# Kernel optimization log

Measured on AMD Instinct MI355X. Metric: run time of the kernel, lower is better.

## Reference

```python
import jax, jax.numpy as jnp
import numpy as np

T, B, V, H, EMB, L = 64, 32, 32000, 1024, 512, 2
PAD, COPY_ID = 0, 3
EPS = 1e-07


def setup_inputs() -> dict:
    key = jax.random.key(0)
    ks = jax.random.split(key, 20)
    s = lambda k, shape, fan: jax.random.normal(k, shape, jnp.float32) / np.sqrt(fan)
    E = s(ks[0], (V, EMB), EMB).at[PAD].set(0.0)  # padding_idx row zero
    return {
        'ref_tokens': jax.random.randint(ks[1], (T, B), 0, V, jnp.int32),
        'h0': jax.random.normal(ks[2], (L, B, H), jnp.float32),
        'c0': jax.random.normal(ks[3], (L, B, H), jnp.float32),
        'E': E,
        'W_ih0': s(ks[4], (4 * H, EMB + H), EMB + H),
        'W_hh0': s(ks[5], (4 * H, H), H),
        'b_ih0': s(ks[6], (4 * H,), H),
        'b_hh0': s(ks[7], (4 * H,), H),
        'W_ih1': s(ks[8], (4 * H, H), H),
        'W_hh1': s(ks[9], (4 * H, H), H),
        'b_ih1': s(ks[10], (4 * H,), H),
        'b_hh1': s(ks[11], (4 * H,), H),
        'Wk': s(ks[12], (H, H), H),
        'bk': s(ks[13], (H,), H),
        'Wc': s(ks[14], (H, 2 * H), 2 * H),
        'bc': s(ks[15], (H,), H),
        'Wp': s(ks[16], (V, H), H),
        'bp': s(ks[17], (V,), H),
    }


def _lstm_cell(x, h, c, Wih, Whh, bih, bhh):
    g = x @ Wih.T + bih + h @ Whh.T + bhh
    i, f, gg, o = jnp.split(g, 4, axis=-1)
    c2 = jax.nn.sigmoid(f) * c + jax.nn.sigmoid(i) * jnp.tanh(gg)
    h2 = jax.nn.sigmoid(o) * jnp.tanh(c2)
    return h2, c2


def _decode(ref_tokens, h0, c0, E, W_ih0, W_hh0, b_ih0, b_hh0,
            W_ih1, W_hh1, b_ih1, b_hh1, Wk, bk, Wc, bc, Wp, bp):
    pad_mask = (ref_tokens == PAD).astype(jnp.float32)      # [T,B]
    b_idx = jnp.broadcast_to(jnp.arange(B)[None, :], (T, B))
    pos = jnp.arange(T)

    def step(carry, xt):
        feed, h, c, hbuf = carry          # feed [B,H], h/c [L,B,H], hbuf [T,B,H]
        tok, t = xt
        emb = E[tok]                      # [B,EMB]
        x = jnp.concatenate([emb, feed], axis=1)
        h0_, c0_ = _lstm_cell(x, h[0], c[0], W_ih0, W_hh0, b_ih0, b_hh0)
        h1_, c1_ = _lstm_cell(h0_, h[1], c[1], W_ih1, W_hh1, b_ih1, b_hh1)
        htop = h1_                        # [B,H]
        hbuf = hbuf.at[t].set(htop)
        # self attention over hiddens 0..t
        keyv = hbuf @ Wk.T + bk           # [T,B,H]
        scores = (keyv * htop[None]).sum(-1) + pad_mask * -99999.0
        scores = jnp.where(pos[:, None] <= t, scores, -1e30)
        dist = jax.nn.softmax(scores, axis=0)          # [T,B]
        summary = (hbuf * dist[:, :, None]).sum(0)     # [B,H]
        comb = jnp.concatenate([htop, summary], axis=1) @ Wc.T + bc  # [B,H]
        pred_logits = comb @ Wp.T + bp                 # [B,V]
        pred_probs = jax.nn.softmax(pred_logits, axis=1)
        copy_probs = jnp.zeros((B, V), jnp.float32).at[(b_idx, ref_tokens)].add(dist) + EPS
        cw = pred_probs[:, COPY_ID:COPY_ID + 1]
        out = jnp.log(cw * copy_probs + (1.0 - cw) * pred_probs)
        new_h = jnp.stack([h0_, h1_])
        new_c = jnp.stack([c0_, c1_])
        return (comb, new_h, new_c, hbuf), out

    init = (jnp.zeros((B, H), jnp.float32), h0, c0, jnp.zeros((T, B, H), jnp.float32))
    (_, hT, cT, _), preds = jax.lax.scan(step, init, (ref_tokens, pos))
    return preds  # [T,B,V]


def reference(ref_tokens, h0, c0, E, W_ih0, W_hh0, b_ih0, b_hh0,
              W_ih1, W_hh1, b_ih1, b_hh1, Wk, bk, Wc, bc, Wp, bp):
    return _decode(ref_tokens, h0, c0, E, W_ih0, W_hh0, b_ih0, b_hh0,
                   W_ih1, W_hh1, b_ih1, b_hh1, Wk, bk, Wc, bc, Wp, bp)
```

## Files before the change

### kernel.cpp

```cpp
#include <hip/hip_runtime.h>
#include <math.h>

#define T_ 64
#define B_ 32
#define V_ 32000
#define H_ 1024
#define EMB_ 512
#define EPS_ 1e-7f
#define COPY_ID_ 3

typedef __bf16 bf16x8 __attribute__((ext_vector_type(8)));
typedef float f32x4 __attribute__((ext_vector_type(4)));

__device__ __forceinline__ unsigned short f2bf(float x) {
    union { float f; unsigned int i; } v; v.f = x;
    unsigned int r = v.i + 0x7FFF + ((v.i >> 16) & 1);
    return (unsigned short)(r >> 16);
}
__device__ __forceinline__ float bf2f(unsigned short h) {
    union { unsigned int i; float f; } v; v.i = ((unsigned int)h) << 16;
    return v.f;
}
__device__ __forceinline__ void f2hilo(float v, unsigned short& h, unsigned short& l) {
    h = f2bf(v);
    l = f2bf(v - bf2f(h));
}

__global__ __launch_bounds__(256) void pack_gates_kernel(
    const float* __restrict__ Wih, int Kih, const float* __restrict__ Whh,
    int Kout, unsigned short* __restrict__ hi, unsigned short* __restrict__ lo)
{
    int idx = blockIdx.x * 256 + threadIdx.x;
    int kq = Kout >> 2;
    int jp = idx / kq;
    if (jp >= 4096) return;
    int k = (idx - jp * kq) << 2;
    int j = (jp & 3) * H_ + (jp >> 2);
    float4 v = (k < Kih) ? *(const float4*)(Wih + (size_t)j * Kih + k)
                         : *(const float4*)(Whh + (size_t)j * H_ + (k - Kih));
    unsigned short h0,l0,h1,l1,h2,l2,h3,l3;
    f2hilo(v.x,h0,l0); f2hilo(v.y,h1,l1); f2hilo(v.z,h2,l2); f2hilo(v.w,h3,l3);
    ushort4 vh; vh.x=h0; vh.y=h1; vh.z=h2; vh.w=h3;
    ushort4 vl; vl.x=l0; vl.y=l1; vl.z=l2; vl.w=l3;
    ((ushort4*)hi)[idx] = vh;
    ((ushort4*)lo)[idx] = vl;
}

__global__ __launch_bounds__(256) void pack_plain_kernel(
    const float* __restrict__ W, unsigned short* __restrict__ hi,
    unsigned short* __restrict__ lo, int n4)
{
    int idx = blockIdx.x * 256 + threadIdx.x;
    if (idx >= n4) return;
    float4 v = ((const float4*)W)[idx];
    unsigned short h0,l0,h1,l1,h2,l2,h3,l3;
    f2hilo(v.x,h0,l0); f2hilo(v.y,h1,l1); f2hilo(v.z,h2,l2); f2hilo(v.w,h3,l3);
    ushort4 vh; vh.x=h0; vh.y=h1; vh.z=h2; vh.w=h3;
    ushort4 vl; vl.x=l0; vl.y=l1; vl.z=l2; vl.w=l3;
    ((ushort4*)hi)[idx] = vh;
    ((ushort4*)lo)[idx] = vl;
}

__global__ __launch_bounds__(256) void embed_hilo_kernel(
    const float* __restrict__ E, const int* __restrict__ tok,
    unsigned short* __restrict__ Xh, unsigned short* __restrict__ Xl)
{
    int idx = blockIdx.x * 256 + threadIdx.x;
    int row = idx >> 7, k = (idx & 127) << 2;
    int tv = tok[row];
    float4 v = *(const float4*)(E + (size_t)tv * EMB_ + k);
    unsigned short h0,l0,h1,l1,h2,l2,h3,l3;
    f2hilo(v.x,h0,l0); f2hilo(v.y,h1,l1); f2hilo(v.z,h2,l2); f2hilo(v.w,h3,l3);
    ushort4 vh; vh.x=h0; vh.y=h1; vh.z=h2; vh.w=h3;
    ushort4 vl; vl.x=l0; vl.y=l1; vl.z=l2; vl.w=l3;
    ((ushort4*)Xh)[idx] = vh;
    ((ushort4*)Xl)[idx] = vl;
}

__global__ __launch_bounds__(256) void init_states_kernel(
    const float* __restrict__ h0i,
    unsigned short* __restrict__ x0h, unsigned short* __restrict__ x0l,
    unsigned short* __restrict__ x1h, unsigned short* __restrict__ x1l)
{
    int idx = blockIdx.x * 256 + threadIdx.x;
    int b = idx >> 10, u = idx & 1023;
    unsigned short h, l;
    x0h[b*2048 + u] = 0; x0l[b*2048 + u] = 0;
    f2hilo(h0i[idx], h, l);
    x0h[b*2048 + 1024 + u] = h; x0l[b*2048 + 1024 + u] = l;
    x1h[b*2048 + u] = 0; x1l[b*2048 + u] = 0;
    f2hilo(h0i[32768 + idx], h, l);
    x1h[b*2048 + 1024 + u] = h; x1l[b*2048 + 1024 + u] = l;
}

template<int K, int XE>
__global__ __launch_bounds__(256) void lstm_mfma_kernel(
    const unsigned short* __restrict__ Xe_h, const unsigned short* __restrict__ Xe_l,
    const unsigned short* __restrict__ Xr_h, const unsigned short* __restrict__ Xr_l,
    const unsigned short* __restrict__ Wh,  const unsigned short* __restrict__ Wl,
    const float* __restrict__ bih, const float* __restrict__ bhh,
    float* __restrict__ c_io,
    unsigned short* __restrict__ d1h, unsigned short* __restrict__ d1l, int d1s, int d1o,
    unsigned short* __restrict__ d2h, unsigned short* __restrict__ d2l, int d2s, int d2o,
    float* __restrict__ hf32)
{
    const int tid = threadIdx.x;
    const int wave = tid >> 6, lane = tid & 63;
    const int quad = lane >> 4, l15 = lane & 15;
    const int n0 = blockIdx.x * 16;
    constexpr int Kq = K >> 2;
    const int kb = wave * Kq;
    const int col = quad * 8;
    f32x4 acc0 = {0.f,0.f,0.f,0.f}, acc1 = {0.f,0.f,0.f,0.f};
    const unsigned short* wrh = Wh + (size_t)(n0 + l15) * K + kb + col;
    const unsigned short* wrl = Wl + (size_t)(n0 + l15) * K + kb + col;
    #pragma unroll 4
    for (int ks = 0; ks < Kq; ks += 32) {
        const int k = kb + ks;
        const unsigned short *ah, *al; int as_;
        if (XE != 0 && k < XE) { ah = Xe_h + k + col; al = Xe_l + k + col; as_ = EMB_; }
        else                   { ah = Xr_h + (k - XE) + col; al = Xr_l + (k - XE) + col; as_ = 2048; }
        bf16x8 a0h = *(const bf16x8*)(ah + l15 * as_);
        bf16x8 a0l = *(const bf16x8*)(al + l15 * as_);
        bf16x8 a1h = *(const bf16x8*)(ah + (16 + l15) * as_);
        bf16x8 a1l = *(const bf16x8*)(al + (16 + l15) * as_);
        bf16x8 bh  = *(const bf16x8*)(wrh + ks);
        bf16x8 bl  = *(const bf16x8*)(wrl + ks);
        acc0 = __builtin_amdgcn_mfma_f32_16x16x32_bf16(a0h, bh, acc0, 0, 0, 0);
        acc1 = __builtin_amdgcn_mfma_f32_16x16x32_bf16(a1h, bh, acc1, 0, 0, 0);
        acc0 = __builtin_amdgcn_mfma_f32_16x16x32_bf16(a0h, bl, acc0, 0, 0, 0);
        acc1 = __builtin_amdgcn_mfma_f32_16x16x32_bf16(a1h, bl, acc1, 0, 0, 0);
        acc0 = __builtin_amdgcn_mfma_f32_16x16x32_bf16(a0l, bh, acc0, 0, 0, 0);
        acc1 = __builtin_amdgcn_mfma_f32_16x16x32_bf16(a1l, bh, acc1, 0, 0, 0);
    }
    __shared__ float Gs[4][32][16];
    __shared__ float Gr[32][16];
    #pragma unroll
    for (int rr = 0; rr < 4; rr++) {
        Gs[wave][quad * 4 + rr][l15]      = acc0[rr];
        Gs[wave][16 + quad * 4 + rr][l15] = acc1[rr];
    }
    __syncthreads();
    #pragma unroll
    for (int it = 0; it < 2; it++) {
        int idx = tid + it * 256;
        int b = idx >> 4, nl = idx & 15;
        float g = Gs[0][b][nl] + Gs[1][b][nl] + Gs[2][b][nl] + Gs[3][b][nl];
        int jn = n0 + nl;
        int j = (jn & 3) * H_ + (jn >> 2);
        Gr[b][nl] = g + bih[j] + bhh[j];
    }
    __syncthreads();
    if (tid < 128) {
        const int b = tid & 31, ul = tid >> 5;
        const int u = (n0 >> 2) + ul;
        const float gi = Gr[b][ul * 4 + 0];
        const float gf = Gr[b][ul * 4 + 1];
        const float gg = Gr[b][ul * 4 + 2];
        const float go = Gr[b][ul * 4 + 3];
        const float cold = c_io[b * H_ + u];
        const float si = 1.f / (1.f + __expf(-gi));
        const float sf = 1.f / (1.f + __expf(-gf));
        const float so = 1.f / (1.f + __expf(-go));
        const float cn = sf * cold + si * tanhf(gg);
        const float hn = so * tanhf(cn);
        c_io[b * H_ + u] = cn;
        unsigned short hh, hl;
        f2hilo(hn, hh, hl);
        d1h[b * d1s + d1o + u] = hh;
        d1l[b * d1s + d1o + u] = hl;
        d2h[b * d2s + d2o + u] = hh;
        d2l[b * d2s + d2o + u] = hl;
        if (hf32) hf32[b * H_ + u] = hn;
    }
}

template<int K, int MODE>
__global__ __launch_bounds__(256) void gemm32_mfma_kernel(
    const unsigned short* __restrict__ Xh, const unsigned short* __restrict__ Xl,
    const unsigned short* __restrict__ Wh, const unsigned short* __restrict__ Wl,
    const float* __restrict__ bias,
    float* __restrict__ outf, unsigned short* __restrict__ outbf,
    unsigned short* __restrict__ dh, unsigned short* __restrict__ dl)
{
    const int tid = threadIdx.x;
    const int wave = tid >> 6, lane = tid & 63;
    const int quad = lane >> 4, l15 = lane & 15;
    const int n0 = blockIdx.x * 16;
    constexpr int Kq = K >> 2;
    const int kb = wave * Kq;
    const int col = quad * 8;
    f32x4 acc0 = {0.f,0.f,0.f,0.f}, acc1 = {0.f,0.f,0.f,0.f};
    const unsigned short* x0h = Xh + (size_t)l15 * K + kb + col;
    const unsigned short* x0l = Xl + (size_t)l15 * K + kb + col;
    const unsigned short* x1h = Xh + (size_t)(16 + l15) * K + kb + col;
    const unsigned short* x1l = Xl + (size_t)(16 + l15) * K + kb + col;
    const unsigned short* wrh = Wh + (size_t)(n0 + l15) * K + kb + col;
    const unsigned short* wrl = Wl + (size_t)(n0 + l15) * K + kb + col;
    #pragma unroll 4
    for (int ks = 0; ks < Kq; ks += 32) {
        bf16x8 a0h = *(const bf16x8*)(x0h + ks);
        bf16x8 a0l = *(const bf16x8*)(x0l + ks);
        bf16x8 a1h = *(const bf16x8*)(x1h + ks);
        bf16x8 a1l = *(const bf16x8*)(x1l + ks);
        bf16x8 bh  = *(const bf16x8*)(wrh + ks);
        bf16x8 bl  = *(const bf16x8*)(wrl + ks);
        acc0 = __builtin_amdgcn_mfma_f32_16x16x32_bf16(a0h, bh, acc0, 0, 0, 0);
        acc1 = __builtin_amdgcn_mfma_f32_16x16x32_bf16(a1h, bh, acc1, 0, 0, 0);
        acc0 = __builtin_amdgcn_mfma_f32_16x16x32_bf16(a0h, bl, acc0, 0, 0, 0);
        acc1 = __builtin_amdgcn_mfma_f32_16x16x32_bf16(a1h, bl, acc1, 0, 0, 0);
        acc0 = __builtin_amdgcn_mfma_f32_16x16x32_bf16(a0l, bh, acc0, 0, 0, 0);
        acc1 = __builtin_amdgcn_mfma_f32_16x16x32_bf16(a1l, bh, acc1, 0, 0, 0);
    }
    __shared__ float Gs[4][32][16];
    #pragma unroll
    for (int rr = 0; rr < 4; rr++) {
        Gs[wave][quad * 4 + rr][l15]      = acc0[rr];
        Gs[wave][16 + quad * 4 + rr][l15] = acc1[rr];
    }
    __syncthreads();
    #pragma unroll
    for (int it = 0; it < 2; it++) {
        int idx = tid + it * 256;
        int b = idx >> 4, nl = idx & 15;
        int n = n0 + nl;
        float v = Gs[0][b][nl] + Gs[1][b][nl] + Gs[2][b][nl] + Gs[3][b][nl] + bias[n];
        if (MODE == 0) {
            outf[b * H_ + n] = v;
        } else {
            outbf[b * H_ + n] = f2bf(v);
            unsigned short hh, hl;
            f2hilo(v, hh, hl);
            dh[b * 2048 + n] = hh;
            dl[b * 2048 + n] = hl;
        }
    }
}

__global__ __launch_bounds__(256) void attn_kernel(
    int t, const float* __restrict__ hbuf, const float* __restrict__ keybuf,
    const int* __restrict__ tokens, float* __restrict__ dist_all,
    unsigned short* __restrict__ cat_h, unsigned short* __restrict__ cat_l)
{
    const int bb = blockIdx.x;
    const int tid = threadIdx.x;
    __shared__ float ht[H_];
    __shared__ float sc[T_];
    __shared__ float dsh[T_];
    for (int k = tid; k < H_; k += 256)
        ht[k] = hbuf[((size_t)t * B_ + bb) * H_ + k];
    __syncthreads();
    const int wave = tid >> 6, lane = tid & 63;
    for (int s = wave; s <= t; s += 4) {
        const float* kv = keybuf + ((size_t)s * B_ + bb) * H_;
        float p = 0.f;
        #pragma unroll
        for (int j = 0; j < 16; j++) p += kv[lane + 64 * j] * ht[lane + 64 * j];
        #pragma unroll
        for (int off = 32; off > 0; off >>= 1) p += __shfl_down(p, off, 64);
        if (lane == 0) {
            float pen = (tokens[s * B_ + bb] == 0) ? -99999.0f : 0.0f;
            sc[s] = p + pen;
        }
    }
    __syncthreads();
    if (tid < 64) {
        float v = (tid <= t) ? sc[tid] : -1e30f;
        float m = v;
        #pragma unroll
        for (int off = 32; off > 0; off >>= 1) m = fmaxf(m, __shfl_down(m, off, 64));
        m = __shfl(m, 0, 64);
        float e = (tid <= t) ? __expf(v - m) : 0.f;
        float ss = e;
        #pragma unroll
        for (int off = 32; off > 0; off >>= 1) ss += __shfl_down(ss, off, 64);
        ss = __shfl(ss, 0, 64);
        float d = e / ss;
        dsh[tid] = d;
        if (tid <= t) dist_all[((size_t)t * T_ + tid) * B_ + bb] = d;
    }
    __syncthreads();
    float sm0 = 0.f, sm1 = 0.f, sm2 = 0.f, sm3 = 0.f;
    for (int s = 0; s <= t; s++) {
        const float d = dsh[s];
        const float* hr = hbuf + ((size_t)s * B_ + bb) * H_;
        sm0 += d * hr[tid];
        sm1 += d * hr[tid + 256];
        sm2 += d * hr[tid + 512];
        sm3 += d * hr[tid + 768];
    }
    const int base = bb * 2048;
    unsigned short hh, hl;
    f2hilo(ht[tid],       hh, hl); cat_h[base + tid]        = hh; cat_l[base + tid]        = hl;
    f2hilo(ht[tid + 256], hh, hl); cat_h[base + tid + 256]  = hh; cat_l[base + tid + 256]  = hl;
    f2hilo(ht[tid + 512], hh, hl); cat_h[base + tid + 512]  = hh; cat_l[base + tid + 512]  = hl;
    f2hilo(ht[tid + 768], hh, hl); cat_h[base + tid + 768]  = hh; cat_l[base + tid + 768]  = hl;
    f2hilo(sm0, hh, hl); cat_h[base + 1024 + tid]       = hh; cat_l[base + 1024 + tid]       = hl;
    f2hilo(sm1, hh, hl); cat_h[base + 1024 + tid + 256] = hh; cat_l[base + 1024 + tid + 256] = hl;
    f2hilo(sm2, hh, hl); cat_h[base + 1024 + tid + 512] = hh; cat_l[base + 1024 + tid + 512] = hl;
    f2hilo(sm3, hh, hl); cat_h[base + 1024 + tid + 768] = hh; cat_l[base + 1024 + tid + 768] = hl;
}

__global__ __launch_bounds__(256) void cast_bf16_kernel(
    const float* __restrict__ src, unsigned short* __restrict__ dst, int n4)
{
    int idx = blockIdx.x * 256 + threadIdx.x;
    int stride = gridDim.x * 256;
    for (int i = idx; i < n4; i += stride) {
        float4 v = ((const float4*)src)[i];
        ushort4 o;
        o.x = f2bf(v.x); o.y = f2bf(v.y); o.z = f2bf(v.z); o.w = f2bf(v.w);
        ((ushort4*)dst)[i] = o;
    }
}

__global__ __launch_bounds__(256) void logits_mfma_kernel(
    const __bf16* __restrict__ Abf, const __bf16* __restrict__ Bbf,
    const float* __restrict__ bp, float* __restrict__ out)
{
    __shared__ __align__(16) __bf16 As[128 * 32];
    __shared__ __align__(16) __bf16 Bs[128 * 32];
    const int tid = threadIdx.x;
    const int lane = tid & 63;
    const int wave = tid >> 6;
    const int quad = lane >> 4, l15 = lane & 15;
    const int m0 = blockIdx.y * 128, n0 = blockIdx.x * 128;
    const int wm = wave >> 1, wn = wave & 1;
    const f32x4 vzero = {0.f, 0.f, 0.f, 0.f};
    f32x4 acc[4][4];
    #pragma unroll
    for (int mt = 0; mt < 4; mt++)
        #pragma unroll
        for (int nt = 0; nt < 4; nt++) acc[mt][nt] = vzero;

    for (int k0 = 0; k0 < 1024; k0 += 32) {
        #pragma unroll
        for (int i = 0; i < 2; i++) {
            int idx = i * 256 + tid;
            int row = idx >> 2, co = (idx & 3) * 8;
            ((uint4*)As)[idx] = *(const uint4*)(Abf + (size_t)(m0 + row) * 1024 + k0 + co);
            ((uint4*)Bs)[idx] = *(const uint4*)(Bbf + (size_t)(n0 + row) * 1024 + k0 + co);
        }
        __syncthreads();
        bf16x8 af[4], bfr[4];
        #pragma unroll
        for (int mt = 0; mt < 4; mt++)
            af[mt] = *(const bf16x8*)&As[(wm * 64 + mt * 16 + l15) * 32 + quad * 8];
        #pragma unroll
        for (int nt = 0; nt < 4; nt++)
            bfr[nt] = *(const bf16x8*)&Bs[(wn * 64 + nt * 16 + l15) * 32 + quad * 8];
        #pragma unroll
        for (int mt = 0; mt < 4; mt++)
            #pragma unroll
            for (int nt = 0; nt < 4; nt++)
                acc[mt][nt] = __builtin_amdgcn_mfma_f32_16x16x32_bf16(
                    af[mt], bfr[nt], acc[mt][nt], 0, 0, 0);
        __syncthreads();
    }
    #pragma unroll
    for (int mt = 0; mt < 4; mt++) {
        #pragma unroll
        for (int nt = 0; nt < 4; nt++) {
            int gcol = n0 + wn * 64 + nt * 16 + l15;
            int growb = m0 + wm * 64 + mt * 16 + quad * 4;
            float bpv = bp[gcol];
            #pragma unroll
            for (int rr = 0; rr < 4; rr++)
                out[(size_t)(growb + rr) * V_ + gcol] = acc[mt][nt][rr] + bpv;
        }
    }
}

__global__ __launch_bounds__(256) void rowstats_kernel(
    const float* __restrict__ logits, float* __restrict__ stats)
{
    const int row = blockIdx.x; const int tid = threadIdx.x;
    const float4* p4 = (const float4*)(logits + (size_t)row * V_);
    __shared__ float red[8];
    const int lane = tid & 63, wave = tid >> 6;
    float m = -1e30f;
    for (int i = tid; i < V_ / 4; i += 256) {
        float4 u = p4[i];
        m = fmaxf(m, fmaxf(fmaxf(u.x, u.y), fmaxf(u.z, u.w)));
    }
    #pragma unroll
    for (int off = 32; off > 0; off >>= 1) m = fmaxf(m, __shfl_down(m, off, 64));
    if (lane == 0) red[wave] = m;
    __syncthreads();
    if (tid == 0) {
        float mm = red[0];
        for (int w = 1; w < 4; w++) mm = fmaxf(mm, red[w]);
        red[4] = mm;
    }
    __syncthreads();
    const float M = red[4];
    float s = 0.f;
    for (int i = tid; i < V_ / 4; i += 256) {
        float4 u = p4[i];
        s += __expf(u.x - M) + __expf(u.y - M) + __expf(u.z - M) + __expf(u.w - M);
    }
    #pragma unroll
    for (int off = 32; off > 0; off >>= 1) s += __shfl_down(s, off, 64);
    if (lane == 0) red[wave] = s;
    __syncthreads();
    if (tid == 0) {
        float S = red[0] + red[1] + red[2] + red[3];
        float lc = logits[(size_t)row * V_ + COPY_ID_];
        float cw = __expf(lc - M) / S;
        stats[row * 4 + 0] = M;
        stats[row * 4 + 1] = S;
        stats[row * 4 + 2] = cw;
    }
}

__global__ __launch_bounds__(64) void fixup_compute_kernel(
    const float* __restrict__ logits, const float* __restrict__ stats,
    const int* __restrict__ tokens, const float* __restrict__ dist_all,
    float* __restrict__ fixval)
{
    const int bid = blockIdx.x;
    const int t = bid >> 5, b = bid & 31;
    const int s = threadIdx.x;
    if (s > t) return;
    const int v = tokens[s * B_ + b];
    float d = 0.f;
    for (int s2 = 0; s2 <= t; s2++)
        if (tokens[s2 * B_ + b] == v)
            d += dist_all[((size_t)t * T_ + s2) * B_ + b];
    const float M = stats[bid * 4], S = stats[bid * 4 + 1], cw = stats[bid * 4 + 2];
    const float l = logits[(size_t)bid * V_ + v];
    const float p = __expf(l - M) / S;
    fixval[((size_t)t * T_ + s) * B_ + b] = __logf(cw * (EPS_ + d) + (1.f - cw) * p);
}

__global__ __launch_bounds__(256) void finalize_kernel(
    float* __restrict__ logits, const float* __restrict__ stats)
{
    const int row = blockIdx.x; const int tid = threadIdx.x;
    float4* p4 = (float4*)(logits + (size_t)row * V_);
    const float M = stats[row * 4], S = stats[row * 4 + 1], cw = stats[row * 4 + 2];
    const float inv = 1.f / S, omc = 1.f - cw, ce = cw * EPS_;
    for (int i = tid; i < V_ / 4; i += 256) {
        float4 u = p4[i];
        u.x = __logf(omc * (__expf(u.x - M) * inv) + ce);
        u.y = __logf(omc * (__expf(u.y - M) * inv) + ce);
        u.z = __logf(omc * (__expf(u.z - M) * inv) + ce);
        u.w = __logf(omc * (__expf(u.w - M) * inv) + ce);
        p4[i] = u;
    }
}

__global__ __launch_bounds__(64) void fixup_apply_kernel(
    float* __restrict__ logits, const int* __restrict__ tokens,
    const float* __restrict__ fixval)
{
    const int bid = blockIdx.x; const int t = bid >> 5, b = bid & 31;
    const int s = threadIdx.x;
    if (s > t) return;
    const int v = tokens[s * B_ + b];
    logits[(size_t)bid * V_ + v] = fixval[((size_t)t * T_ + s) * B_ + b];
}

extern "C" void kernel_launch(void* const* d_in, const int* in_sizes, int n_in,
                              void* d_out, int out_size, void* d_ws, size_t ws_size,
                              hipStream_t stream)
{
    const int*   tok  = (const int*)d_in[0];
    const float* h0i  = (const float*)d_in[1];
    const float* c0i  = (const float*)d_in[2];
    const float* E    = (const float*)d_in[3];
    const float* Wih0 = (const float*)d_in[4];
    const float* Whh0 = (const float*)d_in[5];
    const float* bih0 = (const float*)d_in[6];
    const float* bhh0 = (const float*)d_in[7];
    const float* Wih1 = (const float*)d_in[8];
    const float* Whh1 = (const float*)d_in[9];
    const float* bih1 = (const float*)d_in[10];
    const float* bhh1 = (const float*)d_in[11];
    const float* Wk   = (const float*)d_in[12];
    const float* bk   = (const float*)d_in[13];
    const float* Wc   = (const float*)d_in[14];
    const float* bc   = (const float*)d_in[15];
    const float* Wp   = (const float*)d_in[16];
    const float* bp   = (const float*)d_in[17];
    float* out = (float*)d_out;

    float* ws = (float*)d_ws;
    size_t off = 0;
    float* hbuf   = ws + off; off += (size_t)T_ * B_ * H_;
    float* keybuf = ws + off; off += (size_t)T_ * B_ * H_;
    float* dist   = ws + off; off += (size_t)T_ * T_ * B_;
    float* fixv   = ws + off; off += (size_t)T_ * T_ * B_;
    float* c0b    = ws + off; off += B_ * H_;
    float* c1b    = ws + off; off += B_ * H_;
    float* stats  = ws + off; off += (size_t)T_ * B_ * 4;
    unsigned short* combbf = (unsigned short*)(ws + off); off += (size_t)T_ * B_ * H_ / 2;
    unsigned short* Wpbf   = (unsigned short*)(ws + off); off += (size_t)V_ * H_ / 2;

    unsigned short* os = (unsigned short*)d_out;
    size_t so = 0;
    unsigned short* W0h = os + so; so += (size_t)4096 * 2560;
    unsigned short* W0l = os + so; so += (size_t)4096 * 2560;
    unsigned short* W1h = os + so; so += (size_t)4096 * 2048;
    unsigned short* W1l = os + so; so += (size_t)4096 * 2048;
    unsigned short* Wkh = os + so; so += (size_t)1024 * 1024;
    unsigned short* Wkl = os + so; so += (size_t)1024 * 1024;
    unsigned short* Wch = os + so; so += (size_t)1024 * 2048;
    unsigned short* Wcl = os + so; so += (size_t)1024 * 2048;
    unsigned short* Xeh = os + so; so += (size_t)T_ * B_ * EMB_;
    unsigned short* Xel = os + so; so += (size_t)T_ * B_ * EMB_;
    unsigned short* xr0h = os + so; so += (size_t)2 * B_ * 2048;
    unsigned short* xr0l = os + so; so += (size_t)2 * B_ * 2048;
    unsigned short* xr1h = os + so; so += (size_t)2 * B_ * 2048;
    unsigned short* xr1l = os + so; so += (size_t)2 * B_ * 2048;
    unsigned short* hbh  = os + so; so += (size_t)T_ * B_ * H_;
    unsigned short* hbl  = os + so; so += (size_t)T_ * B_ * H_;
    unsigned short* cath = os + so; so += (size_t)B_ * 2048;
    unsigned short* catl = os + so; so += (size_t)B_ * 2048;

    hipMemcpyAsync(c0b, c0i,           B_ * H_ * 4, hipMemcpyDeviceToDevice, stream);
    hipMemcpyAsync(c1b, c0i + B_ * H_, B_ * H_ * 4, hipMemcpyDeviceToDevice, stream);
    pack_gates_kernel<<<10240, 256, 0, stream>>>(Wih0, 1536, Whh0, 2560, W0h, W0l);
    pack_gates_kernel<<<8192,  256, 0, stream>>>(Wih1, 1024, Whh1, 2048, W1h, W1l);
    pack_plain_kernel<<<1024,  256, 0, stream>>>(Wk, Wkh, Wkl, 1024 * 1024 / 4);
    pack_plain_kernel<<<2048,  256, 0, stream>>>(Wc, Wch, Wcl, 1024 * 2048 / 4);
    embed_hilo_kernel<<<1024,  256, 0, stream>>>(E, tok, Xeh, Xel);
    init_states_kernel<<<128,  256, 0, stream>>>(h0i, xr0h, xr0l, xr1h, xr1l);
    cast_bf16_kernel<<<2048,   256, 0, stream>>>(Wp, Wpbf, V_ * H_ / 4);

    for (int t = 0; t < T_; t++) {
        const size_t cur = (size_t)(t & 1) * B_ * 2048;
        const size_t nxt = (size_t)((t + 1) & 1) * B_ * 2048;
        const size_t to1 = (size_t)t * B_ * H_;
        lstm_mfma_kernel<2560, 512><<<256, 256, 0, stream>>>(
            Xeh + (size_t)t * B_ * EMB_, Xel + (size_t)t * B_ * EMB_,
            xr0h + cur, xr0l + cur, W0h, W0l, bih0, bhh0, c0b,
            xr0h + nxt, xr0l + nxt, 2048, 1024,
            xr1h + cur, xr1l + cur, 2048, 0,
            nullptr);
        lstm_mfma_kernel<2048, 0><<<256, 256, 0, stream>>>(
            xr1h + cur, xr1l + cur,
            xr1h + cur, xr1l + cur, W1h, W1l, bih1, bhh1, c1b,
            xr1h + nxt, xr1l + nxt, 2048, 1024,
            hbh + to1, hbl + to1, 1024, 0,
            hbuf + to1);
        gemm32_mfma_kernel<1024, 0><<<64, 256, 0, stream>>>(
            hbh + to1, hbl + to1, Wkh, Wkl, bk,
            keybuf + to1, nullptr, nullptr, nullptr);
        attn_kernel<<<B_, 256, 0, stream>>>(t, hbuf, keybuf, tok, dist, cath, catl);
        gemm32_mfma_kernel<2048, 1><<<64, 256, 0, stream>>>(
            cath, catl, Wch, Wcl, bc,
            nullptr, combbf + to1, xr0h + nxt, xr0l + nxt);
    }

    dim3 g1(V_ / 128, (T_ * B_) / 128);
    logits_mfma_kernel<<<g1, 256, 0, stream>>>(
        (const __bf16*)combbf, (const __bf16*)Wpbf, bp, out);
    rowstats_kernel<<<T_ * B_, 256, 0, stream>>>(out, stats);
    fixup_compute_kernel<<<T_ * B_, T_, 0, stream>>>(out, stats, tok, dist, fixv);
    finalize_kernel<<<T_ * B_, 256, 0, stream>>>(out, stats);
    fixup_apply_kernel<<<T_ * B_, T_, 0, stream>>>(out, tok, fixv);
}
```

Baseline: 5.544 ms.

## Fuse per-timestep decode loop into one persistent cooperative kernel with grid syncs

Replaces the 64×5 per-step kernel launches with a single cooperative persistent kernel of 256 blocks × 512 threads, using grid-wide syncs between phases. The K-split goes from 4 to 8 waves per block. Attention scores are split out: the key-projection blocks compute the current-step score with an atomic reduction, while the other blocks compute past-step scores in parallel. The summary is then computed across 256 blocks instead of 32. This is meant to cut launch overhead and raise parallelism in the attention step, at the cost of grid-sync latency and a co-residency requirement for all blocks.

```diff
diff --git a/kernel.cpp b/kernel.cpp
--- a/kernel.cpp
+++ b/kernel.cpp
@@ -1,5 +1,8 @@
 #include <hip/hip_runtime.h>
+#include <hip/hip_cooperative_groups.h>
 #include <math.h>
+
+namespace cg = cooperative_groups;
 
 #define T_ 64
 #define B_ 32
@@ -93,22 +96,24 @@
     x1h[b*2048 + 1024 + u] = h; x1l[b*2048 + 1024 + u] = l;
 }
 
+
 template<int K, int XE>
-__global__ __launch_bounds__(256) void lstm_mfma_kernel(
+__device__ __forceinline__ void lstm_phase(
     const unsigned short* __restrict__ Xe_h, const unsigned short* __restrict__ Xe_l,
     const unsigned short* __restrict__ Xr_h, const unsigned short* __restrict__ Xr_l,
     const unsigned short* __restrict__ Wh,  const unsigned short* __restrict__ Wl,
     const float* __restrict__ bih, const float* __restrict__ bhh,
     float* __restrict__ c_io,
-    unsigned short* __restrict__ d1h, unsigned short* __restrict__ d1l, int d1s, int d1o,
-    unsigned short* __restrict__ d2h, unsigned short* __restrict__ d2l, int d2s, int d2o,
-    float* __restrict__ hf32)
+    unsigned short* d1h, unsigned short* d1l, int d1s, int d1o,
+    unsigned short* d2h, unsigned short* d2l, int d2s, int d2o,
+    float* hf32,
+    float (*Gs)[32][16], float (*Gr)[16])
 {
     const int tid = threadIdx.x;
     const int wave = tid >> 6, lane = tid & 63;
     const int quad = lane >> 4, l15 = lane & 15;
     const int n0 = blockIdx.x * 16;
-    constexpr int Kq = K >> 2;
+    constexpr int Kq = K >> 3;
     const int kb = wave * Kq;
     const int col = quad * 8;
     f32x4 acc0 = {0.f,0.f,0.f,0.f}, acc1 = {0.f,0.f,0.f,0.f};
@@ -133,21 +138,19 @@
         acc0 = __builtin_amdgcn_mfma_f32_16x16x32_bf16(a0l, bh, acc0, 0, 0, 0);
         acc1 = __builtin_amdgcn_mfma_f32_16x16x32_bf16(a1l, bh, acc1, 0, 0, 0);
     }
-    __shared__ float Gs[4][32][16];
-    __shared__ float Gr[32][16];
     #pragma unroll
     for (int rr = 0; rr < 4; rr++) {
         Gs[wave][quad * 4 + rr][l15]      = acc0[rr];
         Gs[wave][16 + quad * 4 + rr][l15] = acc1[rr];
     }
     __syncthreads();
-    #pragma unroll
-    for (int it = 0; it < 2; it++) {
-        int idx = tid + it * 256;
-        int b = idx >> 4, nl = idx & 15;
-        float g = Gs[0][b][nl] + Gs[1][b][nl] + Gs[2][b][nl] + Gs[3][b][nl];
-        int jn = n0 + nl;
-        int j = (jn & 3) * H_ + (jn >> 2);
+    {
+        const int b = tid >> 4, nl = tid & 15;
+        float g = 0.f;
+        #pragma unroll
+        for (int w = 0; w < 8; w++) g += Gs[w][b][nl];
+        const int jn = n0 + nl;
+        const int j = (jn & 3) * H_ + (jn >> 2);
         Gr[b][nl] = g + bih[j] + bhh[j];
     }
     __syncthreads();
@@ -176,18 +179,20 @@
 }
 
 template<int K, int MODE>
-__global__ __launch_bounds__(256) void gemm32_mfma_kernel(
+__device__ __forceinline__ void gemm32_phase(
     const unsigned short* __restrict__ Xh, const unsigned short* __restrict__ Xl,
     const unsigned short* __restrict__ Wh, const unsigned short* __restrict__ Wl,
     const float* __restrict__ bias,
-    float* __restrict__ outf, unsigned short* __restrict__ outbf,
-    unsigned short* __restrict__ dh, unsigned short* __restrict__ dl)
+    float* outf, unsigned short* outbf,
+    unsigned short* dh, unsigned short* dl,
+    const float* htop, float* score_row,
+    float (*Gs)[32][16])
 {
     const int tid = threadIdx.x;
     const int wave = tid >> 6, lane = tid & 63;
     const int quad = lane >> 4, l15 = lane & 15;
     const int n0 = blockIdx.x * 16;
-    constexpr int Kq = K >> 2;
+    constexpr int Kq = K >> 3;
     const int kb = wave * Kq;
     const int col = quad * 8;
     f32x4 acc0 = {0.f,0.f,0.f,0.f}, acc1 = {0.f,0.f,0.f,0.f};
@@ -212,21 +217,24 @@
         acc0 = __builtin_amdgcn_mfma_f32_16x16x32_bf16(a0l, bh, acc0, 0, 0, 0);
         acc1 = __builtin_amdgcn_mfma_f32_16x16x32_bf16(a1l, bh, acc1, 0, 0, 0);
     }
-    __shared__ float Gs[4][32][16];
     #pragma unroll
     for (int rr = 0; rr < 4; rr++) {
         Gs[wave][quad * 4 + rr][l15]      = acc0[rr];
         Gs[wave][16 + quad * 4 + rr][l15] = acc1[rr];
     }
     __syncthreads();
-    #pragma unroll
-    for (int it = 0; it < 2; it++) {
-        int idx = tid + it * 256;
-        int b = idx >> 4, nl = idx & 15;
-        int n = n0 + nl;
-        float v = Gs[0][b][nl] + Gs[1][b][nl] + Gs[2][b][nl] + Gs[3][b][nl] + bias[n];
+    {
+        const int b = tid >> 4, nl = tid & 15;
+        const int n = n0 + nl;
+        float v = bias[n];
+        #pragma unroll
+        for (int w = 0; w < 8; w++) v += Gs[w][b][nl];
         if (MODE == 0) {
             outf[b * H_ + n] = v;
+            float pv = v * htop[b * H_ + n];
+            #pragma unroll
+            for (int off = 8; off > 0; off >>= 1) pv += __shfl_down(pv, off, 16);
+            if ((tid & 15) == 0) atomicAdd(score_row + b, pv);
         } else {
             outbf[b * H_ + n] = f2bf(v);
             unsigned short hh, hl;
@@ -237,35 +245,37 @@
     }
 }
 
-__global__ __launch_bounds__(256) void attn_kernel(
+__device__ __forceinline__ void scores_phase(
     int t, const float* __restrict__ hbuf, const float* __restrict__ keybuf,
-    const int* __restrict__ tokens, float* __restrict__ dist_all,
-    unsigned short* __restrict__ cat_h, unsigned short* __restrict__ cat_l)
-{
-    const int bb = blockIdx.x;
+    float* __restrict__ score_g)
+{
+    const int gw = (blockIdx.x - 64) * 8 + (threadIdx.x >> 6);
+    const int lane = threadIdx.x & 63;
+    const float* ht_t = hbuf + (size_t)t * B_ * H_;
+    for (int p = gw; p < t * 32; p += 192 * 8) {
+        const int s = p >> 5, b = p & 31;
+        const float* kv = keybuf + ((size_t)s * B_ + b) * H_;
+        const float* ht = ht_t + (size_t)b * H_;
+        float acc = 0.f;
+        #pragma unroll
+        for (int j = 0; j < 16; j++) acc += kv[lane + 64 * j] * ht[lane + 64 * j];
+        #pragma unroll
+        for (int off = 32; off > 0; off >>= 1) acc += __shfl_down(acc, off, 64);
+        if (lane == 0) score_g[s * 32 + b] = acc;
+    }
+}
+
+__device__ __forceinline__ void attn_phase(
+    int t, const int* __restrict__ tok, const float* __restrict__ hbuf,
+    const float* __restrict__ score_g, float* __restrict__ dist,
+    unsigned short* __restrict__ cath, unsigned short* __restrict__ catl,
+    float* dsh, float (*smp)[128])
+{
+    const int b = blockIdx.x >> 3, slice = blockIdx.x & 7;
     const int tid = threadIdx.x;
-    __shared__ float ht[H_];
-    __shared__ float sc[T_];
-    __shared__ float dsh[T_];
-    for (int k = tid; k < H_; k += 256)
-        ht[k] = hbuf[((size_t)t * B_ + bb) * H_ + k];
-    __syncthreads();
-    const int wave = tid >> 6, lane = tid & 63;
-    for (int s = wave; s <= t; s += 4) {
-        const float* kv = keybuf + ((size_t)s * B_ + bb) * H_;
-        float p = 0.f;
-        #pragma unroll
-        for (int j = 0; j < 16; j++) p += kv[lane + 64 * j] * ht[lane + 64 * j];
-        #pragma unroll
-        for (int off = 32; off > 0; off >>= 1) p += __shfl_down(p, off, 64);
-        if (lane == 0) {
-            float pen = (tokens[s * B_ + bb] == 0) ? -99999.0f : 0.0f;
-            sc[s] = p + pen;
-        }
-    }
-    __syncthreads();
     if (tid < 64) {
-        float v = (tid <= t) ? sc[tid] : -1e30f;
+        float v = (tid <= t) ? score_g[tid * 32 + b] +
+                  ((tok[tid * 32 + b] == 0) ? -99999.0f : 0.0f) : -1e30f;
         float m = v;
         #pragma unroll
         for (int off = 32; off > 0; off >>= 1) m = fmaxf(m, __shfl_down(m, off, 64));
@@ -275,30 +285,86 @@
         #pragma unroll
         for (int off = 32; off > 0; off >>= 1) ss += __shfl_down(ss, off, 64);
         ss = __shfl(ss, 0, 64);
-        float d = e / ss;
-        dsh[tid] = d;
-        if (tid <= t) dist_all[((size_t)t * T_ + tid) * B_ + bb] = d;
-    }
-    __syncthreads();
-    float sm0 = 0.f, sm1 = 0.f, sm2 = 0.f, sm3 = 0.f;
-    for (int s = 0; s <= t; s++) {
-        const float d = dsh[s];
-        const float* hr = hbuf + ((size_t)s * B_ + bb) * H_;
-        sm0 += d * hr[tid];
-        sm1 += d * hr[tid + 256];
-        sm2 += d * hr[tid + 512];
-        sm3 += d * hr[tid + 768];
-    }
-    const int base = bb * 2048;
-    unsigned short hh, hl;
-    f2hilo(ht[tid],       hh, hl); cat_h[base + tid]        = hh; cat_l[base + tid]        = hl;
-    f2hilo(ht[tid + 256], hh, hl); cat_h[base + tid + 256]  = hh; cat_l[base + tid + 256]  = hl;
-    f2hilo(ht[tid + 512], hh, hl); cat_h[base + tid + 512]  = hh; cat_l[base + tid + 512]  = hl;
-    f2hilo(ht[tid + 768], hh, hl); cat_h[base + tid + 768]  = hh; cat_l[base + tid + 768]  = hl;
-    f2hilo(sm0, hh, hl); cat_h[base + 1024 + tid]       = hh; cat_l[base + 1024 + tid]       = hl;
-    f2hilo(sm1, hh, hl); cat_h[base + 1024 + tid + 256] = hh; cat_l[base + 1024 + tid + 256] = hl;
-    f2hilo(sm2, hh, hl); cat_h[base + 1024 + tid + 512] = hh; cat_l[base + 1024 + tid + 512] = hl;
-    f2hilo(sm3, hh, hl); cat_h[base + 1024 + tid + 768] = hh; cat_l[base + 1024 + tid + 768] = hl;
+        dsh[tid] = e / ss;
+    }
+    __syncthreads();
+    const int c = tid & 127, q = tid >> 7;
+    const int col = slice * 128 + c;
+    float sm = 0.f;
+    for (int s = q; s <= t; s += 4)
+        sm += dsh[s] * hbuf[((size_t)s * B_ + b) * H_ + col];
+    smp[q][c] = sm;
+    __syncthreads();
+    if (tid < 128) {
+        const int c2 = slice * 128 + tid;
+        float total = smp[0][tid] + smp[1][tid] + smp[2][tid] + smp[3][tid];
+        unsigned short hh, hl;
+        f2hilo(total, hh, hl);
+        cath[b * 2048 + 1024 + c2] = hh;
+        catl[b * 2048 + 1024 + c2] = hl;
+        const float htv = hbuf[((size_t)t * B_ + b) * H_ + c2];
+        f2hilo(htv, hh, hl);
+        cath[b * 2048 + c2] = hh;
+        catl[b * 2048 + c2] = hl;
+    }
+    if (slice == 0 && tid <= t)
+        dist[((size_t)t * T_ + tid) * B_ + b] = dsh[tid];
+}
+
+struct DecParams {
+    const int* tok;
+    const unsigned short *Xeh, *Xel;
+    unsigned short *xr0h, *xr0l, *xr1h, *xr1l;
+    const unsigned short *W0h, *W0l, *W1h, *W1l, *Wkh, *Wkl, *Wch, *Wcl;
+    const float *bih0, *bhh0, *bih1, *bhh1, *bk, *bc;
+    float *c0b, *c1b;
+    float *hbuf, *keybuf, *score_g, *dist;
+    unsigned short *hbh, *hbl, *cath, *catl, *combbf;
+};
+
+__global__ __launch_bounds__(512) void decode_loop_kernel(DecParams p)
+{
+    cg::grid_group gg = cg::this_grid();
+    __shared__ __align__(16) float Gs[8][32][16];
+    __shared__ float Gr[32][16];
+    __shared__ float dsh[64];
+    __shared__ float smp[4][128];
+    const int blk = blockIdx.x;
+    const int tid = threadIdx.x;
+    for (int t = 0; t < T_; t++) {
+        const size_t cur = (size_t)(t & 1) * B_ * 2048;
+        const size_t nxt = (size_t)((t + 1) & 1) * B_ * 2048;
+        const size_t to1 = (size_t)t * B_ * H_;
+        if (blk == 0 && tid < 32) p.score_g[t * 32 + tid] = 0.f;
+        lstm_phase<2560, 512>(
+            p.Xeh + (size_t)t * B_ * EMB_, p.Xel + (size_t)t * B_ * EMB_,
+            p.xr0h + cur, p.xr0l + cur, p.W0h, p.W0l, p.bih0, p.bhh0, p.c0b,
+            p.xr0h + nxt, p.xr0l + nxt, 2048, 1024,
+            p.xr1h + cur, p.xr1l + cur, 2048, 0,
+            nullptr, Gs, Gr);
+        gg.sync();
+        lstm_phase<2048, 0>(
+            p.xr1h + cur, p.xr1l + cur, p.xr1h + cur, p.xr1l + cur,
+            p.W1h, p.W1l, p.bih1, p.bhh1, p.c1b,
+            p.xr1h + nxt, p.xr1l + nxt, 2048, 1024,
+            p.hbh + to1, p.hbl + to1, 1024, 0,
+            p.hbuf + to1, Gs, Gr);
+        gg.sync();
+        if (blk < 64)
+            gemm32_phase<1024, 0>(p.hbh + to1, p.hbl + to1, p.Wkh, p.Wkl, p.bk,
+                p.keybuf + to1, nullptr, nullptr, nullptr,
+                p.hbuf + to1, p.score_g + t * 32, Gs);
+        else
+            scores_phase(t, p.hbuf, p.keybuf, p.score_g);
+        gg.sync();
+        attn_phase(t, p.tok, p.hbuf, p.score_g, p.dist, p.cath, p.catl, dsh, smp);
+        gg.sync();
+        if (blk < 64)
+            gemm32_phase<2048, 1>(p.cath, p.catl, p.Wch, p.Wcl, p.bc,
+                nullptr, p.combbf + to1, p.xr0h + nxt, p.xr0l + nxt,
+                nullptr, nullptr, Gs);
+        gg.sync();
+    }
 }
 
 __global__ __launch_bounds__(256) void cast_bf16_kernel(
@@ -494,6 +560,7 @@
     float* c0b    = ws + off; off += B_ * H_;
     float* c1b    = ws + off; off += B_ * H_;
     float* stats  = ws + off; off += (size_t)T_ * B_ * 4;
+    float* score_g= ws + off; off += (size_t)T_ * B_;
     unsigned short* combbf = (unsigned short*)(ws + off); off += (size_t)T_ * B_ * H_ / 2;
     unsigned short* Wpbf   = (unsigned short*)(ws + off); off += (size_t)V_ * H_ / 2;
 
@@ -528,30 +595,19 @@
     init_states_kernel<<<128,  256, 0, stream>>>(h0i, xr0h, xr0l, xr1h, xr1l);
     cast_bf16_kernel<<<2048,   256, 0, stream>>>(Wp, Wpbf, V_ * H_ / 4);
 
-    for (int t = 0; t < T_; t++) {
-        const size_t cur = (size_t)(t & 1) * B_ * 2048;
-        const size_t nxt = (size_t)((t + 1) & 1) * B_ * 2048;
-        const size_t to1 = (size_t)t * B_ * H_;
-        lstm_mfma_kernel<2560, 512><<<256, 256, 0, stream>>>(
-            Xeh + (size_t)t * B_ * EMB_, Xel + (size_t)t * B_ * EMB_,
-            xr0h + cur, xr0l + cur, W0h, W0l, bih0, bhh0, c0b,
-            xr0h + nxt, xr0l + nxt, 2048, 1024,
-            xr1h + cur, xr1l + cur, 2048, 0,
-            nullptr);
-        lstm_mfma_kernel<2048, 0><<<256, 256, 0, stream>>>(
-            xr1h + cur, xr1l + cur,
-            xr1h + cur, xr1l + cur, W1h, W1l, bih1, bhh1, c1b,
-            xr1h + nxt, xr1l + nxt, 2048, 1024,
-            hbh + to1, hbl + to1, 1024, 0,
-            hbuf + to1);
-        gemm32_mfma_kernel<1024, 0><<<64, 256, 0, stream>>>(
-            hbh + to1, hbl + to1, Wkh, Wkl, bk,
-            keybuf + to1, nullptr, nullptr, nullptr);
-        attn_kernel<<<B_, 256, 0, stream>>>(t, hbuf, keybuf, tok, dist, cath, catl);
-        gemm32_mfma_kernel<2048, 1><<<64, 256, 0, stream>>>(
-            cath, catl, Wch, Wcl, bc,
-            nullptr, combbf + to1, xr0h + nxt, xr0l + nxt);
-    }
+    DecParams P;
+    P.tok = tok; P.Xeh = Xeh; P.Xel = Xel;
+    P.xr0h = xr0h; P.xr0l = xr0l; P.xr1h = xr1h; P.xr1l = xr1l;
+    P.W0h = W0h; P.W0l = W0l; P.W1h = W1h; P.W1l = W1l;
+    P.Wkh = Wkh; P.Wkl = Wkl; P.Wch = Wch; P.Wcl = Wcl;
+    P.bih0 = bih0; P.bhh0 = bhh0; P.bih1 = bih1; P.bhh1 = bhh1;
+    P.bk = bk; P.bc = bc;
+    P.c0b = c0b; P.c1b = c1b;
+    P.hbuf = hbuf; P.keybuf = keybuf; P.score_g = score_g; P.dist = dist;
+    P.hbh = hbh; P.hbl = hbl; P.cath = cath; P.catl = catl; P.combbf = combbf;
+    void* kargs[] = { (void*)&P };
+    hipLaunchCooperativeKernel(reinterpret_cast<void*>(decode_loop_kernel),
+                               dim3(256), dim3(512), kargs, 0, stream);
 
     dim3 g1(V_ / 128, (T_ * B_) / 128);
     logits_mfma_kernel<<<g1, 256, 0, stream>>>(
```

Result: slower. 13.42 ms (+142.0%).
